# Performance work log

Hardware: AMD Instinct MI355X
Metric: run time of the kernel (lower is better)

Reference implementation:

```python
import jax, jax.numpy as jnp
import numpy as np

B, DIM, H, W = 8, 96, 256, 256
NH, WS, SS = 3, 8, 4
HD = DIM // NH
SCALE = HD ** -0.5
N = WS * WS  # tokens per window


def _rel_pos_log(ws):
    # [N, N, 2] signed log relative coordinates (matches get_relative_positions)
    coords = np.stack(np.meshgrid(np.arange(ws), np.arange(ws), indexing='ij'))
    cf = coords.reshape(2, -1)
    rel = (cf[:, :, None] - cf[:, None, :]).transpose(1, 2, 0).astype(np.float32)
    return np.sign(rel) * np.log1p(np.abs(rel))


def _attn_mask(Hh, Ww, ws, ss):
    # Swin shifted-window mask: [nW, N, N] with 0 / -100
    img = np.zeros((Hh, Ww))
    cnt = 0
    sl = (slice(0, -ws), slice(-ws, -ss), slice(-ss, None))
    for h in sl:
        for w in sl:
            img[h, w] = cnt
            cnt += 1
    mw = img.reshape(Hh // ws, ws, Ww // ws, ws).transpose(0, 2, 1, 3).reshape(-1, ws * ws)
    am = mw[:, None, :] - mw[:, :, None]
    return np.where(am != 0, -100.0, 0.0).astype(np.float32)


REL_POS = jnp.asarray(_rel_pos_log(WS))        # [N, N, 2]
ATTN_MASK = jnp.asarray(_attn_mask(H, W, WS, SS))  # [nW, N, N]


def setup_inputs() -> dict:
    key = jax.random.key(0)
    ks = jax.random.split(key, 8)
    s = 0.02
    return {
        'x': jax.random.normal(ks[0], (B, DIM, H, W), jnp.float32),
        'V_w': jax.random.normal(ks[1], (DIM, DIM), jnp.float32) * s,
        'V_b': jnp.zeros((DIM,), jnp.float32),
        'QK_w': jax.random.normal(ks[2], (2 * DIM, DIM), jnp.float32) * s,
        'QK_b': jnp.zeros((2 * DIM,), jnp.float32),
        'proj_w': jax.random.normal(ks[3], (DIM, DIM), jnp.float32) * s,
        'proj_b': jnp.zeros((DIM,), jnp.float32),
        'dw_w': jax.random.normal(ks[4], (DIM, 5, 5), jnp.float32) * s,
        'dw_b': jnp.zeros((DIM,), jnp.float32),
        'meta_w1': jax.random.normal(ks[5], (256, 2), jnp.float32) * 0.1,
        'meta_b1': jnp.zeros((256,), jnp.float32),
        'meta_w2': jax.random.normal(ks[6], (NH, 256), jnp.float32) * 0.1,
        'meta_b2': jnp.zeros((NH,), jnp.float32),
    }


def reference(x, V_w, V_b, QK_w, QK_b, proj_w, proj_b, dw_w, dw_b,
              meta_w1, meta_b1, meta_w2, meta_b2):
    # 1x1 convs as channel matmuls
    V = jnp.einsum('bchw,oc->bohw', x, V_w) + V_b[None, :, None, None]
    QK = jnp.einsum('bchw,oc->bohw', x, QK_w) + QK_b[None, :, None, None]
    qkv = jnp.concatenate([QK, V], axis=1).transpose(0, 2, 3, 1)  # [B,H,W,3C]
    # cyclic shift
    qkv = jnp.roll(qkv, (-SS, -SS), axis=(1, 2))
    # window partition -> [B*nW, N, 3C]
    xw = qkv.reshape(B, H // WS, WS, W // WS, WS, 3 * DIM)
    xw = xw.transpose(0, 1, 3, 2, 4, 5).reshape(-1, N, 3 * DIM)
    qkv3 = xw.reshape(-1, N, 3, NH, HD).transpose(2, 0, 3, 1, 4)  # [3, B_, nh, N, hd]
    q, k, v = qkv3[0] * SCALE, qkv3[1], qkv3[2]
    attn = jnp.einsum('whnd,whmd->whnm', q, k)  # [B_, nh, N, N]
    # MLP relative-position bias
    bias = jax.nn.relu(REL_POS @ meta_w1.T + meta_b1) @ meta_w2.T + meta_b2  # [N,N,nh]
    attn = attn + bias.transpose(2, 0, 1)[None]
    nW = ATTN_MASK.shape[0]
    attn = attn.reshape(B, nW, NH, N, N) + ATTN_MASK[None, :, None]
    attn = jax.nn.softmax(attn, axis=-1).reshape(-1, NH, N, N)
    xo = jnp.einsum('whnm,whmd->wnhd', attn, v).reshape(-1, N, DIM)
    # window reverse -> [B,H,W,C]
    xr = xo.reshape(B, H // WS, W // WS, WS, WS, DIM)
    xr = xr.transpose(0, 1, 3, 2, 4, 5).reshape(B, H, W, DIM)
    xr = jnp.roll(xr, (SS, SS), axis=(1, 2)).transpose(0, 3, 1, 2)  # [B,C,H,W]
    # depthwise 5x5 conv with reflect padding on V
    Vp = jnp.pad(V, ((0, 0), (0, 0), (2, 2), (2, 2)), mode='reflect')
    conv_out = jax.lax.conv_general_dilated(
        Vp, dw_w.reshape(DIM, 1, 5, 5), (1, 1), 'VALID',
        feature_group_count=DIM,
        dimension_numbers=('NCHW', 'OIHW', 'NCHW')) + dw_b[None, :, None, None]
    out = jnp.einsum('bchw,oc->bohw', conv_out + xr, proj_w) + proj_b[None, :, None, None]
    return out
```

## Files before the change

kernel.cpp:

```cpp
#include <hip/hip_runtime.h>
#include <hip/hip_bf16.h>

#define HW 65536
#define SCALE_Q 0.17677669529663687f

typedef __bf16 bf16x8 __attribute__((ext_vector_type(8)));
typedef float f32x4 __attribute__((ext_vector_type(4)));

__global__ void bias_kernel(const float* __restrict__ w1, const float* __restrict__ b1,
                            const float* __restrict__ w2, const float* __restrict__ b2,
                            float* __restrict__ biasF) {
    int gid = blockIdx.x * blockDim.x + threadIdx.x;
    if (gid >= 12288) return;
    int lane = gid & 63, r = (gid >> 6) & 3, ni = (gid >> 8) & 3, mi = (gid >> 10) & 3, h = gid >> 12;
    int i = mi * 16 + ((lane >> 4) << 2) + r;
    int j = ni * 16 + (lane & 15);
    float di = (float)((i >> 3) - (j >> 3));
    float dj = (float)((i & 7) - (j & 7));
    float r0 = (di > 0.f ? 1.f : (di < 0.f ? -1.f : 0.f)) * log1pf(fabsf(di));
    float r1 = (dj > 0.f ? 1.f : (dj < 0.f ? -1.f : 0.f)) * log1pf(fabsf(dj));
    float acc = 0.f;
    for (int t = 0; t < 256; ++t) {
        float u = fmaf(w1[2 * t], r0, fmaf(w1[2 * t + 1], r1, b1[t]));
        u = fmaxf(u, 0.f);
        acc = fmaf(w2[h * 256 + t], u, acc);
    }
    biasF[gid] = acc + b2[h];
}

__global__ void wtrans_kernel(const float* __restrict__ QK_w, const float* __restrict__ V_w,
                              const float* __restrict__ proj_w,
                              __bf16* __restrict__ Whi, __bf16* __restrict__ Wlo,
                              __bf16* __restrict__ WpHi, __bf16* __restrict__ WpLo) {
    int idx = blockIdx.x * blockDim.x + threadIdx.x;
    if (idx < 288 * 96) {
        int oo = idx / 96, c = idx - oo * 96;
        int h = oo / 96, rem = oo - h * 96, grp = rem >> 5, d = rem & 31;
        float w = (grp == 0) ? QK_w[(h * 32 + d) * 96 + c]
                : (grp == 1) ? QK_w[(96 + h * 32 + d) * 96 + c]
                             : V_w[(h * 32 + d) * 96 + c];
        __bf16 hi = (__bf16)w;
        Whi[idx] = hi;
        Wlo[idx] = (__bf16)(w - (float)hi);
    } else if (idx < 288 * 96 + 96 * 96) {
        int rdx = idx - 288 * 96;
        float w = proj_w[rdx];
        __bf16 hi = (__bf16)w;
        WpHi[rdx] = hi;
        WpLo[rdx] = (__bf16)(w - (float)hi);
    }
}

__global__ __launch_bounds__(256, 3) void fused_qkv_attn(
    const float* __restrict__ x,
    const __bf16* __restrict__ Whi, const __bf16* __restrict__ Wlo,
    const float* __restrict__ QK_b, const float* __restrict__ V_b,
    const float* __restrict__ biasF,
    unsigned short* __restrict__ Vout, float* __restrict__ xr) {
    __shared__ __align__(16) char lds[53376];
    int tid = threadIdx.x;
    int w4 = tid >> 6;
    int lane = tid & 63;
    int l16 = lane & 15;
    int g8 = (lane >> 4) << 3;
    int g4 = (lane >> 4) << 2;
    int bx0 = blockIdx.x;
    int bxs = (bx0 & 7) * 256 + (bx0 >> 3);
    int b = bxs >> 8;
    int wh = (bxs >> 3) & 31;
    int ww0 = (bxs & 7) << 2;
    int wh8 = wh << 3;
    int wb8 = ww0 << 3;
    int ww = ww0 + w4;
    int ti = lane >> 3, tj = lane & 7;
    int ph = (wh8 + ti + 4) & 255;
    int pw = ((ww << 3) + tj + 4) & 255;
    int pos   = ph * 256 + pw;
    int pos_s = (wh8 + ti) * 256 + (ww << 3) + tj;

    __bf16* Xh = (__bf16*)lds;
    const float* xb = x + (size_t)b * 96 * HW;
    for (int idx = tid; idx < 24576; idx += 256) {
        int c = idx >> 8, r = (idx >> 5) & 7, col = idx & 31;
        int pph = (wh8 + r + 4) & 255;
        int ppw = (wb8 + col + 4) & 255;
        Xh[(col >> 3) * 6672 + (r * 8 + (col & 7)) * 104 + c] =
            (__bf16)xb[(size_t)c * HW + pph * 256 + ppw];
    }
    __syncthreads();

    bf16x8 Ah[4][3];
    const __bf16* Xw = Xh + w4 * 6672;
#pragma unroll
    for (int mi = 0; mi < 4; ++mi)
#pragma unroll
        for (int ks = 0; ks < 3; ++ks)
            Ah[mi][ks] = *(const bf16x8*)(Xw + (mi * 16 + l16) * 104 + ks * 32 + g8);
    __syncthreads();

    char* hb = lds + w4 * 9984;
    __bf16* slab = (__bf16*)hb;
    __bf16* Vt   = (__bf16*)(hb + 5120);
    float*  Xr   = (float*)hb;

    bool bhh = (wh == 31), bww = (ww == 31);
    int rc[4];
#pragma unroll
    for (int ni = 0; ni < 4; ++ni) {
        int t = ni * 16 + l16;
        rc[ni] = (bhh ? (((t >> 3) < 4) ? 1 : 2) : 0) * 3 + (bww ? (((t & 7) < 4) ? 1 : 2) : 0);
    }

#pragma unroll 1
    for (int h = 0; h < 3; ++h) {
        bf16x8 Qf[4], Kf[4];
        {
            f32x4 acc[4][2];
#pragma unroll
            for (int mi = 0; mi < 4; ++mi)
#pragma unroll
                for (int ni = 0; ni < 2; ++ni) acc[mi][ni] = (f32x4){0.f, 0.f, 0.f, 0.f};
#pragma unroll
            for (int ks = 0; ks < 3; ++ks)
#pragma unroll
                for (int ni = 0; ni < 2; ++ni) {
                    bf16x8 Bh = *(const bf16x8*)(Whi + (h * 96 + ni * 16 + l16) * 96 + ks * 32 + g8);
#pragma unroll
                    for (int mi = 0; mi < 4; ++mi)
                        acc[mi][ni] = __builtin_amdgcn_mfma_f32_16x16x32_bf16(Ah[mi][ks], Bh, acc[mi][ni], 0, 0, 0);
                }
#pragma unroll
            for (int ni = 0; ni < 2; ++ni) {
                float bias = QK_b[h * 32 + ni * 16 + l16];
#pragma unroll
                for (int mi = 0; mi < 4; ++mi)
#pragma unroll
                    for (int r = 0; r < 4; ++r)
                        slab[(mi * 16 + g4 + r) * 40 + ni * 16 + l16] = (__bf16)((acc[mi][ni][r] + bias) * SCALE_Q);
            }
#pragma unroll
            for (int mi = 0; mi < 4; ++mi) Qf[mi] = *(const bf16x8*)(slab + (mi * 16 + l16) * 40 + g8);
        }
        {
            f32x4 acc[4][2];
#pragma unroll
            for (int mi = 0; mi < 4; ++mi)
#pragma unroll
                for (int ni = 0; ni < 2; ++ni) acc[mi][ni] = (f32x4){0.f, 0.f, 0.f, 0.f};
#pragma unroll
            for (int ks = 0; ks < 3; ++ks)
#pragma unroll
                for (int ni = 0; ni < 2; ++ni) {
                    bf16x8 Bh = *(const bf16x8*)(Whi + (h * 96 + 32 + ni * 16 + l16) * 96 + ks * 32 + g8);
#pragma unroll
                    for (int mi = 0; mi < 4; ++mi)
                        acc[mi][ni] = __builtin_amdgcn_mfma_f32_16x16x32_bf16(Ah[mi][ks], Bh, acc[mi][ni], 0, 0, 0);
                }
#pragma unroll
            for (int ni = 0; ni < 2; ++ni) {
                float bias = QK_b[96 + h * 32 + ni * 16 + l16];
#pragma unroll
                for (int mi = 0; mi < 4; ++mi)
#pragma unroll
                    for (int r = 0; r < 4; ++r)
                        slab[(mi * 16 + g4 + r) * 40 + ni * 16 + l16] = (__bf16)(acc[mi][ni][r] + bias);
            }
#pragma unroll
            for (int mi = 0; mi < 4; ++mi) Kf[mi] = *(const bf16x8*)(slab + (mi * 16 + l16) * 40 + g8);
        }
        {
            f32x4 acc[4][2];
#pragma unroll
            for (int mi = 0; mi < 4; ++mi)
#pragma unroll
                for (int ni = 0; ni < 2; ++ni) acc[mi][ni] = (f32x4){0.f, 0.f, 0.f, 0.f};
#pragma unroll
            for (int ks = 0; ks < 3; ++ks)
#pragma unroll
                for (int ni = 0; ni < 2; ++ni) {
                    int oo = (h * 96 + 64 + ni * 16 + l16) * 96 + ks * 32 + g8;
                    bf16x8 Bh = *(const bf16x8*)(Whi + oo);
                    bf16x8 Bl = *(const bf16x8*)(Wlo + oo);
#pragma unroll
                    for (int mi = 0; mi < 4; ++mi) {
                        acc[mi][ni] = __builtin_amdgcn_mfma_f32_16x16x32_bf16(Ah[mi][ks], Bh, acc[mi][ni], 0, 0, 0);
                        acc[mi][ni] = __builtin_amdgcn_mfma_f32_16x16x32_bf16(Ah[mi][ks], Bl, acc[mi][ni], 0, 0, 0);
                    }
                }
#pragma unroll
            for (int ni = 0; ni < 2; ++ni) {
                float bias = V_b[h * 32 + ni * 16 + l16];
#pragma unroll
                for (int mi = 0; mi < 4; ++mi)
#pragma unroll
                    for (int r = 0; r < 4; ++r)
                        Vt[(ni * 16 + l16) * 72 + mi * 16 + g4 + r] = (__bf16)(acc[mi][ni][r] + bias);
            }
        }
#pragma unroll
        for (int d = 0; d < 32; ++d)
            Vout[(size_t)(b * 96 + h * 32 + d) * HW + pos_s] = ((const unsigned short*)Vt)[d * 72 + lane];

        f32x4 sc[4][4];
#pragma unroll
        for (int mi = 0; mi < 4; ++mi)
#pragma unroll
            for (int ni = 0; ni < 4; ++ni) {
                sc[mi][ni] = (f32x4){0.f, 0.f, 0.f, 0.f};
                sc[mi][ni] = __builtin_amdgcn_mfma_f32_16x16x32_bf16(Qf[mi], Kf[ni], sc[mi][ni], 0, 0, 0);
            }
        const float* bF = biasF + h * 4096;
#pragma unroll
        for (int mi = 0; mi < 4; ++mi)
#pragma unroll
            for (int r = 0; r < 4; ++r) {
                int row = mi * 16 + g4 + r;
                float s0 = sc[mi][0][r] + bF[((mi * 4 + 0) * 4 + r) * 64 + lane];
                float s1 = sc[mi][1][r] + bF[((mi * 4 + 1) * 4 + r) * 64 + lane];
                float s2 = sc[mi][2][r] + bF[((mi * 4 + 2) * 4 + r) * 64 + lane];
                float s3 = sc[mi][3][r] + bF[((mi * 4 + 3) * 4 + r) * 64 + lane];
                if (bhh || bww) {
                    int rr = (bhh ? (((row >> 3) < 4) ? 1 : 2) : 0) * 3 +
                             (bww ? (((row & 7) < 4) ? 1 : 2) : 0);
                    if (rr != rc[0]) s0 -= 100.f;
                    if (rr != rc[1]) s1 -= 100.f;
                    if (rr != rc[2]) s2 -= 100.f;
                    if (rr != rc[3]) s3 -= 100.f;
                }
                float mm = fmaxf(fmaxf(s0, s1), fmaxf(s2, s3));
                mm = fmaxf(mm, __shfl_xor(mm, 1));
                mm = fmaxf(mm, __shfl_xor(mm, 2));
                mm = fmaxf(mm, __shfl_xor(mm, 4));
                mm = fmaxf(mm, __shfl_xor(mm, 8));
                float e0 = __expf(s0 - mm), e1 = __expf(s1 - mm);
                float e2 = __expf(s2 - mm), e3 = __expf(s3 - mm);
                float sum = e0 + e1 + e2 + e3;
                sum += __shfl_xor(sum, 1);
                sum += __shfl_xor(sum, 2);
                sum += __shfl_xor(sum, 4);
                sum += __shfl_xor(sum, 8);
                float inv = 1.f / sum;
                sc[mi][0][r] = e0 * inv;
                sc[mi][1][r] = e1 * inv;
                sc[mi][2][r] = e2 * inv;
                sc[mi][3][r] = e3 * inv;
            }
        f32x4 po[4][2];
#pragma unroll
        for (int mi = 0; mi < 4; ++mi)
#pragma unroll
            for (int ni = 0; ni < 2; ++ni) po[mi][ni] = (f32x4){0.f, 0.f, 0.f, 0.f};
#pragma unroll
        for (int ks = 0; ks < 2; ++ks) {
#pragma unroll
            for (int mi = 0; mi < 4; ++mi)
#pragma unroll
                for (int r = 0; r < 4; ++r) {
                    int row = mi * 16 + g4 + r;
                    slab[row * 40 + l16]      = (__bf16)sc[mi][ks * 2 + 0][r];
                    slab[row * 40 + 16 + l16] = (__bf16)sc[mi][ks * 2 + 1][r];
                }
            bf16x8 Vf[2], Pf;
#pragma unroll
            for (int ni = 0; ni < 2; ++ni)
                Vf[ni] = *(const bf16x8*)(Vt + (ni * 16 + l16) * 72 + ks * 32 + g8);
#pragma unroll
            for (int mi = 0; mi < 4; ++mi) {
                Pf = *(const bf16x8*)(slab + (mi * 16 + l16) * 40 + g8);
#pragma unroll
                for (int ni = 0; ni < 2; ++ni)
                    po[mi][ni] = __builtin_amdgcn_mfma_f32_16x16x32_bf16(Pf, Vf[ni], po[mi][ni], 0, 0, 0);
            }
        }
#pragma unroll
        for (int mi = 0; mi < 4; ++mi)
#pragma unroll
            for (int ni = 0; ni < 2; ++ni)
#pragma unroll
                for (int r = 0; r < 4; ++r)
                    Xr[(mi * 16 + g4 + r) * 36 + ni * 16 + l16] = po[mi][ni][r];
        float* xrg = xr + (size_t)(b * 96 + h * 32) * HW + pos;
#pragma unroll
        for (int c4 = 0; c4 < 8; ++c4) {
            f32x4 v = *(const f32x4*)(Xr + lane * 36 + c4 * 4);
            xrg[(size_t)(c4 * 4 + 0) * HW] = v[0];
            xrg[(size_t)(c4 * 4 + 1) * HW] = v[1];
            xrg[(size_t)(c4 * 4 + 2) * HW] = v[2];
            xrg[(size_t)(c4 * 4 + 3) * HW] = v[3];
        }
    }
}

__global__ __launch_bounds__(256) void dwproj_kernel(
    const __hip_bfloat16* __restrict__ Vs, const float* __restrict__ dw_w,
    const float* __restrict__ dw_b, const __bf16* __restrict__ WpHi,
    const __bf16* __restrict__ WpLo, const float* __restrict__ pb,
    float* __restrict__ T) {
    __shared__ __align__(16) float Ts[12800];
    int bx0 = blockIdx.x;
    int bx = (bx0 & 7) * 512 + (bx0 >> 3);
    int half = bx & 1, h = (bx >> 1) & 255, b = bx >> 9;
    int w0 = half << 7;
    int tid = threadIdx.x;
    for (int task = tid; task < 1536; task += 256) {
        int c = task >> 4, g = task & 15;
        int wbase = w0 + (g << 3);
        const __hip_bfloat16* Vp = Vs + (size_t)(b * 96 + c) * HW;
        const float* wt = dw_w + c * 25;
        float acc[8];
        float bias = dw_b[c];
#pragma unroll
        for (int i = 0; i < 8; ++i) acc[i] = bias;
        bool fast = (wbase >= 8) && (wbase <= 240);
#pragma unroll
        for (int dy = -2; dy <= 2; ++dy) {
            int hh = h + dy;
            hh = hh < 0 ? -hh : (hh > 255 ? 510 - hh : hh);
            int hs = (hh + 252) & 255;
            const __hip_bfloat16* row = Vp + hs * 256;
            float xv[12];
            if (fast) {
                const uint* rp = (const uint*)(row + (wbase - 6));
#pragma unroll
                for (int g2 = 0; g2 < 6; ++g2) {
                    uint u = rp[g2];
                    xv[2 * g2]     = __uint_as_float(u << 16);
                    xv[2 * g2 + 1] = __uint_as_float(u & 0xffff0000u);
                }
            } else {
#pragma unroll
                for (int idx = 0; idx < 12; ++idx) {
                    int cw = wbase - 2 + idx;
                    cw = cw < 0 ? -cw : (cw > 255 ? 510 - cw : cw);
                    int cs = (cw + 252) & 255;
                    uint u = *(const unsigned short*)(row + cs);
                    xv[idx] = __uint_as_float(u << 16);
                }
            }
            const float* w5 = wt + (dy + 2) * 5;
#pragma unroll
            for (int dx = 0; dx < 5; ++dx) {
                float wv = w5[dx];
#pragma unroll
                for (int i = 0; i < 8; ++i) acc[i] = fmaf(wv, xv[i + dx], acc[i]);
            }
        }
        const float* xp = T + (size_t)(b * 96 + c) * HW + h * 256;
        f32x4 x0 = *(const f32x4*)(xp + wbase);
        f32x4 x1 = *(const f32x4*)(xp + wbase + 4);
#pragma unroll
        for (int i = 0; i < 4; ++i) { acc[i] += x0[i]; acc[4 + i] += x1[i]; }
#pragma unroll
        for (int i = 0; i < 8; ++i) Ts[(g * 8 + i) * 100 + c] = acc[i];
    }
    __syncthreads();
    int lane = tid & 63;
    int l16 = lane & 15;
    int g8 = (lane >> 4) << 3;
    int g4 = (lane >> 4) << 2;
    int wv = tid >> 6;
    f32x4 po[2][6];
#pragma unroll
    for (int mi = 0; mi < 2; ++mi)
#pragma unroll
        for (int ni = 0; ni < 6; ++ni) po[mi][ni] = (f32x4){0.f, 0.f, 0.f, 0.f};
#pragma unroll
    for (int ks = 0; ks < 3; ++ks) {
        bf16x8 Ah[2], Al[2];
#pragma unroll
        for (int mi = 0; mi < 2; ++mi) {
            const float* ap = Ts + (wv * 32 + mi * 16 + l16) * 100 + ks * 32 + g8;
            f32x4 a0 = *(const f32x4*)ap;
            f32x4 a1 = *(const f32x4*)(ap + 4);
#pragma unroll
            for (int e = 0; e < 4; ++e) {
                float f0 = a0[e];
                __bf16 h0 = (__bf16)f0;
                Ah[mi][e] = h0;
                Al[mi][e] = (__bf16)(f0 - (float)h0);
                float f1 = a1[e];
                __bf16 h1 = (__bf16)f1;
                Ah[mi][4 + e] = h1;
                Al[mi][4 + e] = (__bf16)(f1 - (float)h1);
            }
        }
#pragma unroll
        for (int ni = 0; ni < 6; ++ni) {
            int o = ni * 16 + l16;
            bf16x8 Bh = *(const bf16x8*)(WpHi + o * 96 + ks * 32 + g8);
            bf16x8 Bl = *(const bf16x8*)(WpLo + o * 96 + ks * 32 + g8);
#pragma unroll
            for (int mi = 0; mi < 2; ++mi) {
                po[mi][ni] = __builtin_amdgcn_mfma_f32_16x16x32_bf16(Ah[mi], Bh, po[mi][ni], 0, 0, 0);
                po[mi][ni] = __builtin_amdgcn_mfma_f32_16x16x32_bf16(Al[mi], Bh, po[mi][ni], 0, 0, 0);
                po[mi][ni] = __builtin_amdgcn_mfma_f32_16x16x32_bf16(Ah[mi], Bl, po[mi][ni], 0, 0, 0);
            }
        }
    }
#pragma unroll
    for (int ni = 0; ni < 6; ++ni) {
        int o = ni * 16 + l16;
        float bias = pb[o];
#pragma unroll
        for (int mi = 0; mi < 2; ++mi) {
            f32x4 v = po[mi][ni];
            v[0] += bias; v[1] += bias; v[2] += bias; v[3] += bias;
            *(f32x4*)(T + (size_t)(b * 96 + o) * HW + h * 256 + w0 + wv * 32 + mi * 16 + g4) = v;
        }
    }
}

extern "C" void kernel_launch(void* const* d_in, const int* in_sizes, int n_in,
                              void* d_out, int out_size, void* d_ws, size_t ws_size,
                              hipStream_t stream) {
    const float* x      = (const float*)d_in[0];
    const float* V_w    = (const float*)d_in[1];
    const float* V_b    = (const float*)d_in[2];
    const float* QK_w   = (const float*)d_in[3];
    const float* QK_b   = (const float*)d_in[4];
    const float* proj_w = (const float*)d_in[5];
    const float* proj_b = (const float*)d_in[6];
    const float* dw_w   = (const float*)d_in[7];
    const float* dw_b   = (const float*)d_in[8];
    const float* mw1    = (const float*)d_in[9];
    const float* mb1    = (const float*)d_in[10];
    const float* mw2    = (const float*)d_in[11];
    const float* mb2    = (const float*)d_in[12];
    float* out = (float*)d_out;

    char* ws = (char*)d_ws;
    __hip_bfloat16* Vbuf = (__hip_bfloat16*)ws;
    float*  biasF = (float*)(ws + 100663296);
    __bf16* Whi   = (__bf16*)(ws + 100663296 + 49152);
    __bf16* Wlo   = (__bf16*)(ws + 100663296 + 49152 + 55296);
    __bf16* WpHi  = (__bf16*)(ws + 100663296 + 49152 + 2 * 55296);
    __bf16* WpLo  = (__bf16*)(ws + 100663296 + 49152 + 2 * 55296 + 18432);

    bias_kernel<<<48, 256, 0, stream>>>(mw1, mb1, mw2, mb2, biasF);
    wtrans_kernel<<<144, 256, 0, stream>>>(QK_w, V_w, proj_w, Whi, Wlo, WpHi, WpLo);
    fused_qkv_attn<<<2048, 256, 0, stream>>>(x, Whi, Wlo, QK_b, V_b, biasF,
                                             (unsigned short*)Vbuf, out);
    dwproj_kernel<<<4096, 256, 0, stream>>>(Vbuf, dw_w, dw_b, WpHi, WpLo, proj_b, out);
}
```

Measured before the change: 724.7 us.

## Shrink LDS footprints to raise occupancy in attention and dwproj kernels

The attention kernel now stages the input tile in two channel chunks (64 then 32) instead of all 96 at once. This cuts shared memory from about 53KB to 40KB, and the launch bound is raised to 4 blocks per CU. The dwproj kernel processes 64-pixel quarter rows instead of half rows, halving its LDS and accumulator registers and doubling the grid to 8192 blocks with a 5-block occupancy target. The trade-off is extra barriers and a second global staging pass in attention, plus more blocks that each reload proj weights in dwproj.

```diff
diff --git a/kernel.cpp b/kernel.cpp
--- a/kernel.cpp
+++ b/kernel.cpp
@@ -51,13 +51,13 @@
     }
 }
 
-__global__ __launch_bounds__(256, 3) void fused_qkv_attn(
+__global__ __launch_bounds__(256, 4) void fused_qkv_attn(
     const float* __restrict__ x,
     const __bf16* __restrict__ Whi, const __bf16* __restrict__ Wlo,
     const float* __restrict__ QK_b, const float* __restrict__ V_b,
     const float* __restrict__ biasF,
     unsigned short* __restrict__ Vout, float* __restrict__ xr) {
-    __shared__ __align__(16) char lds[53376];
+    __shared__ __align__(16) char lds[39936];
     int tid = threadIdx.x;
     int w4 = tid >> 6;
     int lane = tid & 63;
@@ -78,25 +78,42 @@
     int pos   = ph * 256 + pw;
     int pos_s = (wh8 + ti) * 256 + (ww << 3) + tj;
 
-    __bf16* Xh = (__bf16*)lds;
     const float* xb = x + (size_t)b * 96 * HW;
-    for (int idx = tid; idx < 24576; idx += 256) {
-        int c = idx >> 8, r = (idx >> 5) & 7, col = idx & 31;
-        int pph = (wh8 + r + 4) & 255;
-        int ppw = (wb8 + col + 4) & 255;
-        Xh[(col >> 3) * 6672 + (r * 8 + (col & 7)) * 104 + c] =
-            (__bf16)xb[(size_t)c * HW + pph * 256 + ppw];
-    }
-    __syncthreads();
-
     bf16x8 Ah[4][3];
-    const __bf16* Xw = Xh + w4 * 6672;
-#pragma unroll
-    for (int mi = 0; mi < 4; ++mi)
-#pragma unroll
-        for (int ks = 0; ks < 3; ++ks)
-            Ah[mi][ks] = *(const bf16x8*)(Xw + (mi * 16 + l16) * 104 + ks * 32 + g8);
-    __syncthreads();
+    {
+        __bf16* XA = (__bf16*)lds;
+        for (int idx = tid; idx < 16384; idx += 256) {
+            int c = idx >> 8, r = (idx >> 5) & 7, col = idx & 31;
+            int pph = (wh8 + r + 4) & 255;
+            int ppw = (wb8 + col + 4) & 255;
+            XA[(col >> 3) * 4608 + ((r << 3) + (col & 7)) * 72 + c] =
+                (__bf16)xb[(size_t)c * HW + pph * 256 + ppw];
+        }
+        __syncthreads();
+        const __bf16* Xw = XA + w4 * 4608;
+#pragma unroll
+        for (int mi = 0; mi < 4; ++mi) {
+            Ah[mi][0] = *(const bf16x8*)(Xw + (mi * 16 + l16) * 72 + g8);
+            Ah[mi][1] = *(const bf16x8*)(Xw + (mi * 16 + l16) * 72 + 32 + g8);
+        }
+        __syncthreads();
+    }
+    {
+        __bf16* XB = (__bf16*)lds;
+        for (int idx = tid; idx < 8192; idx += 256) {
+            int c = idx >> 8, r = (idx >> 5) & 7, col = idx & 31;
+            int pph = (wh8 + r + 4) & 255;
+            int ppw = (wb8 + col + 4) & 255;
+            XB[(col >> 3) * 2560 + ((r << 3) + (col & 7)) * 40 + c] =
+                (__bf16)xb[(size_t)(64 + c) * HW + pph * 256 + ppw];
+        }
+        __syncthreads();
+        const __bf16* Xw2 = (const __bf16*)lds + w4 * 2560;
+#pragma unroll
+        for (int mi = 0; mi < 4; ++mi)
+            Ah[mi][2] = *(const bf16x8*)(Xw2 + (mi * 16 + l16) * 40 + g8);
+        __syncthreads();
+    }
 
     char* hb = lds + w4 * 9984;
     __bf16* slab = (__bf16*)hb;
@@ -291,19 +308,19 @@
     }
 }
 
-__global__ __launch_bounds__(256) void dwproj_kernel(
+__global__ __launch_bounds__(256, 5) void dwproj_kernel(
     const __hip_bfloat16* __restrict__ Vs, const float* __restrict__ dw_w,
     const float* __restrict__ dw_b, const __bf16* __restrict__ WpHi,
     const __bf16* __restrict__ WpLo, const float* __restrict__ pb,
     float* __restrict__ T) {
-    __shared__ __align__(16) float Ts[12800];
+    __shared__ __align__(16) float Ts[6400];
     int bx0 = blockIdx.x;
-    int bx = (bx0 & 7) * 512 + (bx0 >> 3);
-    int half = bx & 1, h = (bx >> 1) & 255, b = bx >> 9;
-    int w0 = half << 7;
+    int bxs = (bx0 & 7) * 1024 + (bx0 >> 3);
+    int q = bxs & 3, h = (bxs >> 2) & 255, b = bxs >> 10;
+    int w0 = q << 6;
     int tid = threadIdx.x;
-    for (int task = tid; task < 1536; task += 256) {
-        int c = task >> 4, g = task & 15;
+    for (int task = tid; task < 768; task += 256) {
+        int c = task >> 3, g = task & 7;
         int wbase = w0 + (g << 3);
         const __hip_bfloat16* Vp = Vs + (size_t)(b * 96 + c) * HW;
         const float* wt = dw_w + c * 25;
@@ -351,7 +368,7 @@
 #pragma unroll
         for (int i = 0; i < 4; ++i) { acc[i] += x0[i]; acc[4 + i] += x1[i]; }
 #pragma unroll
-        for (int i = 0; i < 8; ++i) Ts[(g * 8 + i) * 100 + c] = acc[i];
+        for (int i = 0; i < 8; ++i) Ts[((g << 3) + i) * 100 + c] = acc[i];
     }
     __syncthreads();
     int lane = tid & 63;
@@ -359,54 +376,43 @@
     int g8 = (lane >> 4) << 3;
     int g4 = (lane >> 4) << 2;
     int wv = tid >> 6;
-    f32x4 po[2][6];
-#pragma unroll
-    for (int mi = 0; mi < 2; ++mi)
-#pragma unroll
-        for (int ni = 0; ni < 6; ++ni) po[mi][ni] = (f32x4){0.f, 0.f, 0.f, 0.f};
+    f32x4 po[6];
+#pragma unroll
+    for (int ni = 0; ni < 6; ++ni) po[ni] = (f32x4){0.f, 0.f, 0.f, 0.f};
 #pragma unroll
     for (int ks = 0; ks < 3; ++ks) {
-        bf16x8 Ah[2], Al[2];
-#pragma unroll
-        for (int mi = 0; mi < 2; ++mi) {
-            const float* ap = Ts + (wv * 32 + mi * 16 + l16) * 100 + ks * 32 + g8;
-            f32x4 a0 = *(const f32x4*)ap;
-            f32x4 a1 = *(const f32x4*)(ap + 4);
-#pragma unroll
-            for (int e = 0; e < 4; ++e) {
-                float f0 = a0[e];
-                __bf16 h0 = (__bf16)f0;
-                Ah[mi][e] = h0;
-                Al[mi][e] = (__bf16)(f0 - (float)h0);
-                float f1 = a1[e];
-                __bf16 h1 = (__bf16)f1;
-                Ah[mi][4 + e] = h1;
-                Al[mi][4 + e] = (__bf16)(f1 - (float)h1);
-            }
+        bf16x8 Ah, Al;
+        const float* ap = Ts + (wv * 16 + l16) * 100 + ks * 32 + g8;
+        f32x4 a0 = *(const f32x4*)ap;
+        f32x4 a1 = *(const f32x4*)(ap + 4);
+#pragma unroll
+        for (int e = 0; e < 4; ++e) {
+            float f0 = a0[e];
+            __bf16 h0 = (__bf16)f0;
+            Ah[e] = h0;
+            Al[e] = (__bf16)(f0 - (float)h0);
+            float f1 = a1[e];
+            __bf16 h1 = (__bf16)f1;
+            Ah[4 + e] = h1;
+            Al[4 + e] = (__bf16)(f1 - (float)h1);
         }
 #pragma unroll
         for (int ni = 0; ni < 6; ++ni) {
             int o = ni * 16 + l16;
             bf16x8 Bh = *(const bf16x8*)(WpHi + o * 96 + ks * 32 + g8);
             bf16x8 Bl = *(const bf16x8*)(WpLo + o * 96 + ks * 32 + g8);
-#pragma unroll
-            for (int mi = 0; mi < 2; ++mi) {
-                po[mi][ni] = __builtin_amdgcn_mfma_f32_16x16x32_bf16(Ah[mi], Bh, po[mi][ni], 0, 0, 0);
-                po[mi][ni] = __builtin_amdgcn_mfma_f32_16x16x32_bf16(Al[mi], Bh, po[mi][ni], 0, 0, 0);
-                po[mi][ni] = __builtin_amdgcn_mfma_f32_16x16x32_bf16(Ah[mi], Bl, po[mi][ni], 0, 0, 0);
-            }
+            po[ni] = __builtin_amdgcn_mfma_f32_16x16x32_bf16(Ah, Bh, po[ni], 0, 0, 0);
+            po[ni] = __builtin_amdgcn_mfma_f32_16x16x32_bf16(Al, Bh, po[ni], 0, 0, 0);
+            po[ni] = __builtin_amdgcn_mfma_f32_16x16x32_bf16(Ah, Bl, po[ni], 0, 0, 0);
         }
     }
 #pragma unroll
     for (int ni = 0; ni < 6; ++ni) {
         int o = ni * 16 + l16;
         float bias = pb[o];
-#pragma unroll
-        for (int mi = 0; mi < 2; ++mi) {
-            f32x4 v = po[mi][ni];
-            v[0] += bias; v[1] += bias; v[2] += bias; v[3] += bias;
-            *(f32x4*)(T + (size_t)(b * 96 + o) * HW + h * 256 + w0 + wv * 32 + mi * 16 + g4) = v;
-        }
+        f32x4 v = po[ni];
+        v[0] += bias; v[1] += bias; v[2] += bias; v[3] += bias;
+        *(f32x4*)(T + (size_t)(b * 96 + o) * HW + h * 256 + w0 + wv * 16 + g4) = v;
     }
 }
 
@@ -440,5 +446,5 @@
     wtrans_kernel<<<144, 256, 0, stream>>>(QK_w, V_w, proj_w, Whi, Wlo, WpHi, WpLo);
     fused_qkv_attn<<<2048, 256, 0, stream>>>(x, Whi, Wlo, QK_b, V_b, biasF,
                                              (unsigned short*)Vbuf, out);
-    dwproj_kernel<<<4096, 256, 0, stream>>>(Vbuf, dw_w, dw_b, WpHi, WpLo, proj_b, out);
+    dwproj_kernel<<<8192, 256, 0, stream>>>(Vbuf, dw_w, dw_b, WpHi, WpLo, proj_b, out);
 }
```

Result: slower. 960.3 us (+32.5%).
